# Optimization experiments

Measured on AMD Instinct MI355X. Metric: run time of the kernel, lower is better.

## Reference

```python
import jax, jax.numpy as jnp
import numpy as np

N = 1_000_000          # query points
L = 6                  # positional encoding terms
ND = 3                 # n_dims
C = 16                 # n_features
G = 96                 # feature grid resolution per axis
NODES = 128            # decoder width
IN_DIM = C + L * ND * 2  # 52
VOL_MIN, VOL_MAX = 0.0, 1.0


def setup_inputs() -> dict:
    key = jax.random.key(0)
    ks = jax.random.split(key, 8)
    x = jax.random.uniform(ks[0], (N, ND), jnp.float32, minval=-1.0, maxval=1.0)
    feature_grid = jax.random.uniform(ks[1], (C, G, G, G), jnp.float32)  # torch.rand init
    s = 0.05
    w_in = jax.random.normal(ks[2], (IN_DIM, NODES), jnp.float32) * s
    w_h0 = jax.random.normal(ks[3], (NODES, NODES), jnp.float32) * s
    w_h1 = jax.random.normal(ks[4], (NODES, NODES), jnp.float32) * s
    w_h2 = jax.random.normal(ks[5], (NODES, NODES), jnp.float32) * s
    w_out = jax.random.normal(ks[6], (NODES, 1), jnp.float32) * s
    return {"x": x, "feature_grid": feature_grid, "w_in": w_in,
            "w_h0": w_h0, "w_h1": w_h1, "w_h2": w_h2, "w_out": w_out}


def _trilinear(grid, pts):
    """grid_sample 3D, bilinear, align_corners=True. grid [C,D,H,W], pts [N,3]
    with channel order (x->W, y->H, z->D) as in torch. Returns [N, C]."""
    Cc, D, H, W = grid.shape
    fx = (pts[:, 0] + 1.0) * 0.5 * (W - 1)
    fy = (pts[:, 1] + 1.0) * 0.5 * (H - 1)
    fz = (pts[:, 2] + 1.0) * 0.5 * (D - 1)
    x0 = jnp.floor(fx); y0 = jnp.floor(fy); z0 = jnp.floor(fz)
    tx = fx - x0; ty = fy - y0; tz = fz - z0
    x0i = jnp.clip(x0.astype(jnp.int32), 0, W - 1); x1i = jnp.clip(x0i + 1, 0, W - 1)
    y0i = jnp.clip(y0.astype(jnp.int32), 0, H - 1); y1i = jnp.clip(y0i + 1, 0, H - 1)
    z0i = jnp.clip(z0.astype(jnp.int32), 0, D - 1); z1i = jnp.clip(z0i + 1, 0, D - 1)

    def g(zi, yi, xi):
        return grid[:, zi, yi, xi].T  # [N, C]

    c000 = g(z0i, y0i, x0i); c001 = g(z0i, y0i, x1i)
    c010 = g(z0i, y1i, x0i); c011 = g(z0i, y1i, x1i)
    c100 = g(z1i, y0i, x0i); c101 = g(z1i, y0i, x1i)
    c110 = g(z1i, y1i, x0i); c111 = g(z1i, y1i, x1i)
    tx = tx[:, None]; ty = ty[:, None]; tz = tz[:, None]
    c00 = c000 * (1 - tx) + c001 * tx
    c01 = c010 * (1 - tx) + c011 * tx
    c10 = c100 * (1 - tx) + c101 * tx
    c11 = c110 * (1 - tx) + c111 * tx
    c0 = c00 * (1 - ty) + c01 * ty
    c1 = c10 * (1 - ty) + c11 * ty
    return c0 * (1 - tz) + c1 * tz


def _pos_enc(pts):
    # [N, L*ND*2]: sin/cos of pi * 2^k * x for k in 0..L-1
    freqs = (jnp.pi * (2.0 ** jnp.arange(L, dtype=jnp.float32)))  # [L]
    ang = pts[:, None, :] * freqs[None, :, None]                   # [N, L, ND]
    pe = jnp.concatenate([jnp.sin(ang), jnp.cos(ang)], axis=-1)    # [N, L, 2*ND]
    return pe.reshape(pts.shape[0], -1)


def reference(x, feature_grid, w_in, w_h0, w_h1, w_h2, w_out):
    feats = _trilinear(feature_grid, x)          # [N, C]
    pe = _pos_enc(x)                             # [N, 2*L*ND]
    h = jnp.concatenate([pe, feats], axis=1)     # [N, IN_DIM]
    h = jax.nn.relu(h @ w_in)
    h = jax.nn.relu(h @ w_h0)
    h = jax.nn.relu(h @ w_h1)
    h = jax.nn.relu(h @ w_h2)
    y = h @ w_out                                # [N, 1]
    return y * (VOL_MAX - VOL_MIN) + VOL_MIN
```

## Files before the change

kernel.cpp:

```cpp
#include <hip/hip_runtime.h>
#include <stdint.h>

typedef unsigned int uint;
typedef unsigned short ushort;

#define GD   96
#define GD2  (GD*GD)
#define GSP  (GD*GD*GD)
#define NPTS 1000000
#define WIN_ELTS 8192
#define WH_ELTS  16384
#define WFRAG_OFF (GSP*16)

#define PW   128
#define ROWB 272
#define LDS_BYTES (4*PW*ROWB)

typedef __attribute__((ext_vector_type(8))) short short8;
typedef __attribute__((ext_vector_type(4))) float f32x4;

__device__ __forceinline__ uint f2bf(float x) {
  uint u = __float_as_uint(x);
  return (u + 0x7fffu + ((u >> 16) & 1u)) >> 16;
}

__global__ void k_grid_pack(const float* __restrict__ g, ushort* __restrict__ o) {
  int sp = blockIdx.x * 256 + threadIdx.x;
  uint pk[8];
#pragma unroll
  for (int c = 0; c < 16; c += 2) {
    float a = g[(size_t)c * GSP + sp];
    float b = g[(size_t)(c + 1) * GSP + sp];
    pk[c >> 1] = f2bf(a) | (f2bf(b) << 16);
  }
  uint4* dst = (uint4*)(o + (size_t)sp * 16);
  dst[0] = make_uint4(pk[0], pk[1], pk[2], pk[3]);
  dst[1] = make_uint4(pk[4], pk[5], pk[6], pk[7]);
}

__global__ void k_w_pack(const float* __restrict__ win, const float* __restrict__ h0,
                         const float* __restrict__ h1, const float* __restrict__ h2,
                         ushort* __restrict__ o) {
  int tid = blockIdx.x * 256 + threadIdx.x;
  int lane = (tid >> 3) & 63, j = tid & 7;
  int q = lane >> 4, cc = lane & 15;
  float v;
  if (tid < WIN_ELTS) {
    int blk = tid >> 9;
    int t = blk >> 1, s = blk & 1;
    int k = s * 32 + q * 8 + j, n = t * 16 + cc;
    v = (k < 52) ? win[k * 128 + n] : 0.f;
  } else {
    int f2 = tid - WIN_ELTS;
    int l = f2 >> 14, r = f2 & 16383;
    int blk = r >> 9;
    int t = blk >> 2, s = blk & 3;
    int k = s * 32 + q * 8 + j, n = t * 16 + cc;
    const float* w = (l == 0) ? h0 : ((l == 1) ? h1 : h2);
    v = w[k * 128 + n];
  }
  o[tid] = (ushort)f2bf(v);
}

#define ACC8(off, U, W) {                                  \
  fv[(off)+0] += (W) * __uint_as_float((U).x << 16);       \
  fv[(off)+1] += (W) * __uint_as_float((U).x & 0xffff0000u);\
  fv[(off)+2] += (W) * __uint_as_float((U).y << 16);       \
  fv[(off)+3] += (W) * __uint_as_float((U).y & 0xffff0000u);\
  fv[(off)+4] += (W) * __uint_as_float((U).z << 16);       \
  fv[(off)+5] += (W) * __uint_as_float((U).z & 0xffff0000u);\
  fv[(off)+6] += (W) * __uint_as_float((U).w << 16);       \
  fv[(off)+7] += (W) * __uint_as_float((U).w & 0xffff0000u);\
}

#define MFMA(A,B,C) __builtin_amdgcn_mfma_f32_16x16x32_bf16((A),(B),(C),0,0,0)

__global__ __launch_bounds__(256, 1) void k_main(
    const float* __restrict__ x, const float* __restrict__ wout,
    const ushort* __restrict__ gridb, const ushort* __restrict__ wfrag,
    float* __restrict__ out) {
  extern __shared__ char smem[];
  const int wave = threadIdx.x >> 6;
  const int lane = threadIdx.x & 63;
  const int q = lane >> 4, c = lane & 15;
  char* act = smem + wave * (PW * ROWB);
  const int base = blockIdx.x * (4 * PW) + wave * PW;

#pragma unroll
  for (int pp = 0; pp < 2; ++pp) {
    const int p = pp * 64 + lane;
    const int gp = base + p;
    const int gpc = min(gp, NPTS - 1);
    const float px = x[gpc * 3 + 0];
    const float py = x[gpc * 3 + 1];
    const float pz = x[gpc * 3 + 2];
    float fx = (px + 1.0f) * 0.5f * 95.0f;
    float fy = (py + 1.0f) * 0.5f * 95.0f;
    float fz = (pz + 1.0f) * 0.5f * 95.0f;
    float x0f = floorf(fx), y0f = floorf(fy), z0f = floorf(fz);
    float tx = fx - x0f, ty = fy - y0f, tz = fz - z0f;
    int x0i = min(max((int)x0f, 0), 95);
    int y0i = min(max((int)y0f, 0), 95);
    int z0i = min(max((int)z0f, 0), 95);
    int x1i = min(x0i + 1, 95);
    int y1i = min(y0i + 1, 95);
    int z1i = min(z0i + 1, 95);
    float fv[16];
#pragma unroll
    for (int k = 0; k < 16; ++k) fv[k] = 0.f;
#pragma unroll
    for (int dz = 0; dz < 2; ++dz) {
      const int zi = dz ? z1i : z0i;
      const float wz = dz ? tz : (1.f - tz);
#pragma unroll
      for (int dy = 0; dy < 2; ++dy) {
        const int yi = dy ? y1i : y0i;
        const float wzy = wz * (dy ? ty : (1.f - ty));
        const ushort* r0 = gridb + (size_t)(zi * GD2 + yi * GD + x0i) * 16;
        const ushort* r1 = gridb + (size_t)(zi * GD2 + yi * GD + x1i) * 16;
        uint4 a0 = *(const uint4*)r0;
        uint4 a1 = *(const uint4*)(r0 + 8);
        uint4 b0 = *(const uint4*)r1;
        uint4 b1 = *(const uint4*)(r1 + 8);
        const float w0 = wzy * (1.f - tx), w1 = wzy * tx;
        ACC8(0, a0, w0); ACC8(8, a1, w0);
        ACC8(0, b0, w1); ACC8(8, b1, w1);
      }
    }
    float row[64];
#pragma unroll
    for (int i = 0; i < 6; ++i) {
      const float fr = 3.14159265358979323846f * (float)(1 << i);
      row[i*6+0] = __sinf(px*fr); row[i*6+1] = __sinf(py*fr); row[i*6+2] = __sinf(pz*fr);
      row[i*6+3] = __cosf(px*fr); row[i*6+4] = __cosf(py*fr); row[i*6+5] = __cosf(pz*fr);
    }
#pragma unroll
    for (int k = 0; k < 16; ++k) row[36 + k] = fv[k];
#pragma unroll
    for (int k = 52; k < 64; ++k) row[k] = 0.f;
    char* dst = act + p * ROWB;
#pragma unroll
    for (int k = 0; k < 64; k += 8) {
      uint u0 = f2bf(row[k+0]) | (f2bf(row[k+1]) << 16);
      uint u1 = f2bf(row[k+2]) | (f2bf(row[k+3]) << 16);
      uint u2 = f2bf(row[k+4]) | (f2bf(row[k+5]) << 16);
      uint u3 = f2bf(row[k+6]) | (f2bf(row[k+7]) << 16);
      *(uint4*)(dst + k * 2) = make_uint4(u0, u1, u2, u3);
    }
  }
  asm volatile("s_waitcnt lgkmcnt(0)" ::: "memory");

  {
    short8 bw[16];
#pragma unroll
    for (int f = 0; f < 16; ++f)
      bw[f] = *(const short8*)(wfrag + f * 512 + lane * 8);
    const char* ar0 = act + c * ROWB + q * 16;
    short8 a0 = *(const short8*)(ar0);
    short8 a1 = *(const short8*)(ar0 + 64);
    for (int mt = 0; mt < 8; ++mt) {
      const short8 ca0 = a0, ca1 = a1;
      if (mt < 7) {
        const char* arn = act + ((mt + 1) * 16 + c) * ROWB + q * 16;
        a0 = *(const short8*)(arn);
        a1 = *(const short8*)(arn + 64);
      }
      f32x4 av[8];
#pragma unroll
      for (int t = 0; t < 8; ++t) av[t] = f32x4{0.f, 0.f, 0.f, 0.f};
#pragma unroll
      for (int t = 0; t < 8; ++t) {
        av[t] = MFMA(ca0, bw[t*2+0], av[t]);
        av[t] = MFMA(ca1, bw[t*2+1], av[t]);
      }
      asm volatile("s_waitcnt lgkmcnt(0)" ::: "memory");
      char* yb = act + (mt * 16 + q * 4) * ROWB + c * 2;
#pragma unroll
      for (int t = 0; t < 8; ++t)
#pragma unroll
        for (int r = 0; r < 4; ++r)
          *(ushort*)(yb + r * ROWB + t * 32) = (ushort)f2bf(fmaxf(av[t][r], 0.f));
    }
  }
  asm volatile("s_waitcnt lgkmcnt(0)" ::: "memory");

  for (int l = 0; l < 3; ++l) {
    const ushort* wl = wfrag + WIN_ELTS + l * WH_ELTS;
    short8 bw[32];
#pragma unroll
    for (int f = 0; f < 32; ++f)
      bw[f] = *(const short8*)(wl + f * 512 + lane * 8);
    if (l < 2) {
      const char* ar0 = act + c * ROWB + q * 16;
      short8 a0 = *(const short8*)(ar0);
      short8 a1 = *(const short8*)(ar0 + 64);
      short8 a2 = *(const short8*)(ar0 + 128);
      short8 a3 = *(const short8*)(ar0 + 192);
      for (int mt = 0; mt < 8; ++mt) {
        const short8 ca0 = a0, ca1 = a1, ca2 = a2, ca3 = a3;
        if (mt < 7) {
          const char* arn = act + ((mt + 1) * 16 + c) * ROWB + q * 16;
          a0 = *(const short8*)(arn);
          a1 = *(const short8*)(arn + 64);
          a2 = *(const short8*)(arn + 128);
          a3 = *(const short8*)(arn + 192);
        }
        f32x4 av[8];
#pragma unroll
        for (int t = 0; t < 8; ++t) av[t] = f32x4{0.f, 0.f, 0.f, 0.f};
#pragma unroll
        for (int t = 0; t < 8; ++t) {
          av[t] = MFMA(ca0, bw[t*4+0], av[t]);
          av[t] = MFMA(ca1, bw[t*4+1], av[t]);
          av[t] = MFMA(ca2, bw[t*4+2], av[t]);
          av[t] = MFMA(ca3, bw[t*4+3], av[t]);
        }
        asm volatile("s_waitcnt lgkmcnt(0)" ::: "memory");
        char* yb = act + (mt * 16 + q * 4) * ROWB + c * 2;
#pragma unroll
        for (int t = 0; t < 8; ++t)
#pragma unroll
          for (int r = 0; r < 4; ++r)
            *(ushort*)(yb + r * ROWB + t * 32) = (ushort)f2bf(fmaxf(av[t][r], 0.f));
      }
      asm volatile("s_waitcnt lgkmcnt(0)" ::: "memory");
    } else {
      float wo[8];
#pragma unroll
      for (int t = 0; t < 8; ++t) wo[t] = wout[t * 16 + c];
      const char* ar0 = act + c * ROWB + q * 16;
      short8 a0 = *(const short8*)(ar0);
      short8 a1 = *(const short8*)(ar0 + 64);
      short8 a2 = *(const short8*)(ar0 + 128);
      short8 a3 = *(const short8*)(ar0 + 192);
      for (int mt = 0; mt < 8; ++mt) {
        const short8 ca0 = a0, ca1 = a1, ca2 = a2, ca3 = a3;
        if (mt < 7) {
          const char* arn = act + ((mt + 1) * 16 + c) * ROWB + q * 16;
          a0 = *(const short8*)(arn);
          a1 = *(const short8*)(arn + 64);
          a2 = *(const short8*)(arn + 128);
          a3 = *(const short8*)(arn + 192);
        }
        f32x4 av[8];
#pragma unroll
        for (int t = 0; t < 8; ++t) av[t] = f32x4{0.f, 0.f, 0.f, 0.f};
#pragma unroll
        for (int t = 0; t < 8; ++t) {
          av[t] = MFMA(ca0, bw[t*4+0], av[t]);
          av[t] = MFMA(ca1, bw[t*4+1], av[t]);
          av[t] = MFMA(ca2, bw[t*4+2], av[t]);
          av[t] = MFMA(ca3, bw[t*4+3], av[t]);
        }
#pragma unroll
        for (int r = 0; r < 4; ++r) {
          float y = 0.f;
#pragma unroll
          for (int t = 0; t < 8; ++t) y += fmaxf(av[t][r], 0.f) * wo[t];
          y += __shfl_xor(y, 1, 64);
          y += __shfl_xor(y, 2, 64);
          y += __shfl_xor(y, 4, 64);
          y += __shfl_xor(y, 8, 64);
          if (c == r) {
            int gpo = base + mt * 16 + q * 4 + r;
            if (gpo < NPTS) out[gpo] = y;
          }
        }
      }
    }
  }
}

extern "C" void kernel_launch(void* const* d_in, const int* in_sizes, int n_in,
                              void* d_out, int out_size, void* d_ws, size_t ws_size,
                              hipStream_t stream) {
  const float* x    = (const float*)d_in[0];
  const float* fg   = (const float*)d_in[1];
  const float* win  = (const float*)d_in[2];
  const float* wh0  = (const float*)d_in[3];
  const float* wh1  = (const float*)d_in[4];
  const float* wh2  = (const float*)d_in[5];
  const float* wout = (const float*)d_in[6];
  float* out = (float*)d_out;

  ushort* gridb = (ushort*)d_ws;
  ushort* wfrag = (ushort*)d_ws + WFRAG_OFF;

  k_grid_pack<<<GSP / 256, 256, 0, stream>>>(fg, gridb);
  k_w_pack<<<(WIN_ELTS + 3 * WH_ELTS) / 256, 256, 0, stream>>>(win, wh0, wh1, wh2, wfrag);

  const int nblk = (NPTS + 4 * PW - 1) / (4 * PW);
  k_main<<<nblk, 256, LDS_BYTES, stream>>>(x, wout, gridb, wfrag, out);
}
```

Before: 394.9 us.

## Split trilinear gather and encoding into a separate kernel feeding the MLP

```diff
diff --git a/kernel.cpp b/kernel.cpp
--- a/kernel.cpp
+++ b/kernel.cpp
@@ -11,10 +11,13 @@
 #define WIN_ELTS 8192
 #define WH_ELTS  16384
 #define WFRAG_OFF (GSP*16)
+#define WFRAG_N  (WIN_ELTS + 3*WH_ELTS)
+#define ACT_OFF  (WFRAG_OFF + WFRAG_N)
 
 #define PW   128
 #define ROWB 272
 #define LDS_BYTES (4*PW*ROWB)
+#define NROWS (1954*512)
 
 typedef __attribute__((ext_vector_type(8))) short short8;
 typedef __attribute__((ext_vector_type(4))) float f32x4;
@@ -73,12 +76,72 @@
   fv[(off)+7] += (W) * __uint_as_float((U).w & 0xffff0000u);\
 }
 
+__global__ void k_gather(const float* __restrict__ x,
+                         const ushort* __restrict__ gridb,
+                         ushort* __restrict__ actg) {
+  const int p = blockIdx.x * 256 + threadIdx.x;
+  if (p >= NROWS) return;
+  const int pc = min(p, NPTS - 1);
+  const float px = x[pc * 3 + 0];
+  const float py = x[pc * 3 + 1];
+  const float pz = x[pc * 3 + 2];
+  float fx = (px + 1.0f) * 0.5f * 95.0f;
+  float fy = (py + 1.0f) * 0.5f * 95.0f;
+  float fz = (pz + 1.0f) * 0.5f * 95.0f;
+  float x0f = floorf(fx), y0f = floorf(fy), z0f = floorf(fz);
+  float tx = fx - x0f, ty = fy - y0f, tz = fz - z0f;
+  int x0i = min(max((int)x0f, 0), 95);
+  int y0i = min(max((int)y0f, 0), 95);
+  int z0i = min(max((int)z0f, 0), 95);
+  int x1i = min(x0i + 1, 95);
+  int y1i = min(y0i + 1, 95);
+  int z1i = min(z0i + 1, 95);
+  float fv[16];
+#pragma unroll
+  for (int k = 0; k < 16; ++k) fv[k] = 0.f;
+#pragma unroll
+  for (int dz = 0; dz < 2; ++dz) {
+    const int zi = dz ? z1i : z0i;
+    const float wz = dz ? tz : (1.f - tz);
+#pragma unroll
+    for (int dy = 0; dy < 2; ++dy) {
+      const int yi = dy ? y1i : y0i;
+      const float wzy = wz * (dy ? ty : (1.f - ty));
+      const ushort* r0 = gridb + (size_t)(zi * GD2 + yi * GD + x0i) * 16;
+      const ushort* r1 = gridb + (size_t)(zi * GD2 + yi * GD + x1i) * 16;
+      uint4 a0 = *(const uint4*)r0;
+      uint4 a1 = *(const uint4*)(r0 + 8);
+      uint4 b0 = *(const uint4*)r1;
+      uint4 b1 = *(const uint4*)(r1 + 8);
+      const float w0 = wzy * (1.f - tx), w1 = wzy * tx;
+      ACC8(0, a0, w0); ACC8(8, a1, w0);
+      ACC8(0, b0, w1); ACC8(8, b1, w1);
+    }
+  }
+  uint pk[32];
+#pragma unroll
+  for (int i = 0; i < 6; ++i) {
+    const float fr = 3.14159265358979323846f * (float)(1 << i);
+    pk[i*3+0] = f2bf(__sinf(px*fr)) | (f2bf(__sinf(py*fr)) << 16);
+    pk[i*3+1] = f2bf(__sinf(pz*fr)) | (f2bf(__cosf(px*fr)) << 16);
+    pk[i*3+2] = f2bf(__cosf(py*fr)) | (f2bf(__cosf(pz*fr)) << 16);
+  }
+#pragma unroll
+  for (int j = 0; j < 8; ++j)
+    pk[18+j] = f2bf(fv[2*j]) | (f2bf(fv[2*j+1]) << 16);
+#pragma unroll
+  for (int j = 26; j < 32; ++j) pk[j] = 0u;
+  uint4* dst = (uint4*)(actg + (size_t)p * 64);
+#pragma unroll
+  for (int k = 0; k < 8; ++k)
+    dst[k] = make_uint4(pk[4*k+0], pk[4*k+1], pk[4*k+2], pk[4*k+3]);
+}
+
 #define MFMA(A,B,C) __builtin_amdgcn_mfma_f32_16x16x32_bf16((A),(B),(C),0,0,0)
 
-__global__ __launch_bounds__(256, 1) void k_main(
-    const float* __restrict__ x, const float* __restrict__ wout,
-    const ushort* __restrict__ gridb, const ushort* __restrict__ wfrag,
-    float* __restrict__ out) {
+__global__ __launch_bounds__(256, 1) void k_mlp(
+    const ushort* __restrict__ actg, const float* __restrict__ wout,
+    const ushort* __restrict__ wfrag, float* __restrict__ out) {
   extern __shared__ char smem[];
   const int wave = threadIdx.x >> 6;
   const int lane = threadIdx.x & 63;
@@ -86,84 +149,20 @@
   char* act = smem + wave * (PW * ROWB);
   const int base = blockIdx.x * (4 * PW) + wave * PW;
 
-#pragma unroll
-  for (int pp = 0; pp < 2; ++pp) {
-    const int p = pp * 64 + lane;
-    const int gp = base + p;
-    const int gpc = min(gp, NPTS - 1);
-    const float px = x[gpc * 3 + 0];
-    const float py = x[gpc * 3 + 1];
-    const float pz = x[gpc * 3 + 2];
-    float fx = (px + 1.0f) * 0.5f * 95.0f;
-    float fy = (py + 1.0f) * 0.5f * 95.0f;
-    float fz = (pz + 1.0f) * 0.5f * 95.0f;
-    float x0f = floorf(fx), y0f = floorf(fy), z0f = floorf(fz);
-    float tx = fx - x0f, ty = fy - y0f, tz = fz - z0f;
-    int x0i = min(max((int)x0f, 0), 95);
-    int y0i = min(max((int)y0f, 0), 95);
-    int z0i = min(max((int)z0f, 0), 95);
-    int x1i = min(x0i + 1, 95);
-    int y1i = min(y0i + 1, 95);
-    int z1i = min(z0i + 1, 95);
-    float fv[16];
-#pragma unroll
-    for (int k = 0; k < 16; ++k) fv[k] = 0.f;
-#pragma unroll
-    for (int dz = 0; dz < 2; ++dz) {
-      const int zi = dz ? z1i : z0i;
-      const float wz = dz ? tz : (1.f - tz);
-#pragma unroll
-      for (int dy = 0; dy < 2; ++dy) {
-        const int yi = dy ? y1i : y0i;
-        const float wzy = wz * (dy ? ty : (1.f - ty));
-        const ushort* r0 = gridb + (size_t)(zi * GD2 + yi * GD + x0i) * 16;
-        const ushort* r1 = gridb + (size_t)(zi * GD2 + yi * GD + x1i) * 16;
-        uint4 a0 = *(const uint4*)r0;
-        uint4 a1 = *(const uint4*)(r0 + 8);
-        uint4 b0 = *(const uint4*)r1;
-        uint4 b1 = *(const uint4*)(r1 + 8);
-        const float w0 = wzy * (1.f - tx), w1 = wzy * tx;
-        ACC8(0, a0, w0); ACC8(8, a1, w0);
-        ACC8(0, b0, w1); ACC8(8, b1, w1);
-      }
-    }
-    float row[64];
-#pragma unroll
-    for (int i = 0; i < 6; ++i) {
-      const float fr = 3.14159265358979323846f * (float)(1 << i);
-      row[i*6+0] = __sinf(px*fr); row[i*6+1] = __sinf(py*fr); row[i*6+2] = __sinf(pz*fr);
-      row[i*6+3] = __cosf(px*fr); row[i*6+4] = __cosf(py*fr); row[i*6+5] = __cosf(pz*fr);
-    }
-#pragma unroll
-    for (int k = 0; k < 16; ++k) row[36 + k] = fv[k];
-#pragma unroll
-    for (int k = 52; k < 64; ++k) row[k] = 0.f;
-    char* dst = act + p * ROWB;
-#pragma unroll
-    for (int k = 0; k < 64; k += 8) {
-      uint u0 = f2bf(row[k+0]) | (f2bf(row[k+1]) << 16);
-      uint u1 = f2bf(row[k+2]) | (f2bf(row[k+3]) << 16);
-      uint u2 = f2bf(row[k+4]) | (f2bf(row[k+5]) << 16);
-      uint u3 = f2bf(row[k+6]) | (f2bf(row[k+7]) << 16);
-      *(uint4*)(dst + k * 2) = make_uint4(u0, u1, u2, u3);
-    }
-  }
-  asm volatile("s_waitcnt lgkmcnt(0)" ::: "memory");
-
   {
     short8 bw[16];
 #pragma unroll
     for (int f = 0; f < 16; ++f)
       bw[f] = *(const short8*)(wfrag + f * 512 + lane * 8);
-    const char* ar0 = act + c * ROWB + q * 16;
-    short8 a0 = *(const short8*)(ar0);
-    short8 a1 = *(const short8*)(ar0 + 64);
+    const ushort* ag = actg + (size_t)(base + c) * 64 + q * 8;
+    short8 a0 = *(const short8*)(ag);
+    short8 a1 = *(const short8*)(ag + 32);
     for (int mt = 0; mt < 8; ++mt) {
       const short8 ca0 = a0, ca1 = a1;
       if (mt < 7) {
-        const char* arn = act + ((mt + 1) * 16 + c) * ROWB + q * 16;
-        a0 = *(const short8*)(arn);
-        a1 = *(const short8*)(arn + 64);
+        const ushort* an = ag + (size_t)(mt + 1) * 16 * 64;
+        a0 = *(const short8*)(an);
+        a1 = *(const short8*)(an + 32);
       }
       f32x4 av[8];
 #pragma unroll
@@ -285,10 +284,12 @@
 
   ushort* gridb = (ushort*)d_ws;
   ushort* wfrag = (ushort*)d_ws + WFRAG_OFF;
+  ushort* actg  = (ushort*)d_ws + ACT_OFF;
 
   k_grid_pack<<<GSP / 256, 256, 0, stream>>>(fg, gridb);
   k_w_pack<<<(WIN_ELTS + 3 * WH_ELTS) / 256, 256, 0, stream>>>(win, wh0, wh1, wh2, wfrag);
+  k_gather<<<NROWS / 256, 256, 0, stream>>>(x, gridb, actg);
 
   const int nblk = (NPTS + 4 * PW - 1) / (4 * PW);
-  k_main<<<nblk, 256, LDS_BYTES, stream>>>(x, wout, gridb, wfrag, out);
-}
+  k_mlp<<<nblk, 256, LDS_BYTES, stream>>>(actg, wout, wfrag, out);
+}
```

Result: slower. 512.4 us (+29.7%).

## Bin query points into z-slabs before main kernel for gather locality

Applied to the files above, without the earlier changes.

```diff
diff --git a/kernel.cpp b/kernel.cpp
--- a/kernel.cpp
+++ b/kernel.cpp
@@ -11,6 +11,16 @@
 #define WIN_ELTS 8192
 #define WH_ELTS  16384
 #define WFRAG_OFF (GSP*16)
+#define WFRAG_N  (WIN_ELTS + 3*WH_ELTS)
+
+#define NSLAB 8
+#define SLABZ 12
+#define CAP   131072
+#define NSLOT (NSLAB*CAP)
+
+#define XS_BYTE   ((size_t)(WFRAG_OFF + WFRAG_N) * 2)
+#define OID_BYTE  (XS_BYTE + (size_t)NSLOT * 16)
+#define CUR_BYTE  (OID_BYTE + (size_t)NSLOT * 4)
 
 #define PW   128
 #define ROWB 272
@@ -62,6 +72,49 @@
   o[tid] = (ushort)f2bf(v);
 }
 
+__global__ void k_prefill(const float* __restrict__ x, float4* __restrict__ xs,
+                          int* __restrict__ oid, int* __restrict__ cursor) {
+  int id = blockIdx.x * 256 + threadIdx.x;
+  float lx = x[(NPTS - 1) * 3 + 0];
+  float ly = x[(NPTS - 1) * 3 + 1];
+  float lz = x[(NPTS - 1) * 3 + 2];
+  xs[id] = make_float4(lx, ly, lz, 0.f);
+  oid[id] = NPTS - 1;
+  if (id < NSLAB) cursor[id] = id * CAP;
+}
+
+__global__ void k_scatter(const float* __restrict__ x, float4* __restrict__ xs,
+                          int* __restrict__ oid, int* __restrict__ cursor) {
+  __shared__ int lc[NSLAB], lb[NSLAB];
+  const int tid = threadIdx.x;
+  if (tid < NSLAB) lc[tid] = 0;
+  __syncthreads();
+  const int pbase = blockIdx.x * 4096;
+  int rk[16], sl[16];
+#pragma unroll
+  for (int i = 0; i < 16; ++i) {
+    int p = pbase + i * 256 + tid;
+    int pc = min(p, NPTS - 1);
+    float pz = x[pc * 3 + 2];
+    int z0i = min(max((int)floorf((pz + 1.0f) * 0.5f * 95.0f), 0), 95);
+    int s = z0i / SLABZ;
+    sl[i] = s;
+    rk[i] = (p < NPTS) ? atomicAdd(&lc[s], 1) : -1;
+  }
+  __syncthreads();
+  if (tid < NSLAB) lb[tid] = atomicAdd(&cursor[tid], lc[tid]);
+  __syncthreads();
+#pragma unroll
+  for (int i = 0; i < 16; ++i) {
+    int p = pbase + i * 256 + tid;
+    if (p < NPTS) {
+      int slot = lb[sl[i]] + rk[i];
+      xs[slot] = make_float4(x[p * 3 + 0], x[p * 3 + 1], x[p * 3 + 2], 0.f);
+      oid[slot] = p;
+    }
+  }
+}
+
 #define ACC8(off, U, W) {                                  \
   fv[(off)+0] += (W) * __uint_as_float((U).x << 16);       \
   fv[(off)+1] += (W) * __uint_as_float((U).x & 0xffff0000u);\
@@ -76,7 +129,8 @@
 #define MFMA(A,B,C) __builtin_amdgcn_mfma_f32_16x16x32_bf16((A),(B),(C),0,0,0)
 
 __global__ __launch_bounds__(256, 1) void k_main(
-    const float* __restrict__ x, const float* __restrict__ wout,
+    const float4* __restrict__ xs, const int* __restrict__ oid,
+    const float* __restrict__ wout,
     const ushort* __restrict__ gridb, const ushort* __restrict__ wfrag,
     float* __restrict__ out) {
   extern __shared__ char smem[];
@@ -84,16 +138,16 @@
   const int lane = threadIdx.x & 63;
   const int q = lane >> 4, c = lane & 15;
   char* act = smem + wave * (PW * ROWB);
-  const int base = blockIdx.x * (4 * PW) + wave * PW;
+  const int b = blockIdx.x;
+  const int base = (b & 7) * CAP + (b >> 3) * 512 + wave * PW;
 
 #pragma unroll
   for (int pp = 0; pp < 2; ++pp) {
     const int p = pp * 64 + lane;
-    const int gp = base + p;
-    const int gpc = min(gp, NPTS - 1);
-    const float px = x[gpc * 3 + 0];
-    const float py = x[gpc * 3 + 1];
-    const float pz = x[gpc * 3 + 2];
+    const float4 c4 = xs[base + p];
+    const float px = c4.x;
+    const float py = c4.y;
+    const float pz = c4.z;
     float fx = (px + 1.0f) * 0.5f * 95.0f;
     float fy = (py + 1.0f) * 0.5f * 95.0f;
     float fz = (pz + 1.0f) * 0.5f * 95.0f;
@@ -262,8 +316,8 @@
           y += __shfl_xor(y, 4, 64);
           y += __shfl_xor(y, 8, 64);
           if (c == r) {
-            int gpo = base + mt * 16 + q * 4 + r;
-            if (gpo < NPTS) out[gpo] = y;
+            int slot = base + mt * 16 + q * 4 + r;
+            out[oid[slot]] = y;
           }
         }
       }
@@ -283,12 +337,17 @@
   const float* wout = (const float*)d_in[6];
   float* out = (float*)d_out;
 
-  ushort* gridb = (ushort*)d_ws;
-  ushort* wfrag = (ushort*)d_ws + WFRAG_OFF;
+  char* wsb = (char*)d_ws;
+  ushort* gridb  = (ushort*)d_ws;
+  ushort* wfrag  = (ushort*)d_ws + WFRAG_OFF;
+  float4* xs     = (float4*)(wsb + XS_BYTE);
+  int*    oid    = (int*)(wsb + OID_BYTE);
+  int*    cursor = (int*)(wsb + CUR_BYTE);
 
   k_grid_pack<<<GSP / 256, 256, 0, stream>>>(fg, gridb);
   k_w_pack<<<(WIN_ELTS + 3 * WH_ELTS) / 256, 256, 0, stream>>>(win, wh0, wh1, wh2, wfrag);
-
-  const int nblk = (NPTS + 4 * PW - 1) / (4 * PW);
-  k_main<<<nblk, 256, LDS_BYTES, stream>>>(x, wout, gridb, wfrag, out);
-}
+  k_prefill<<<NSLOT / 256, 256, 0, stream>>>(x, xs, oid, cursor);
+  k_scatter<<<(NPTS + 4095) / 4096, 256, 0, stream>>>(x, xs, oid, cursor);
+
+  k_main<<<NSLAB * (CAP / 512), 256, LDS_BYTES, stream>>>(xs, oid, wout, gridb, wfrag, out);
+}
```

After: 411.2 us. 4.1% more time.
